# Kernel optimization log

Hardware: AMD Instinct MI355X
Metric: run time of the kernel (lower is better)

Reference implementation:

```python
import jax, jax.numpy as jnp
import numpy as np

NUM_PROJS = 7
BLOCK_SIZE = 256   # key block size
SAMPLE_SIZE = 256  # residual sampled keys


def _gray_perm(n):
    # AngularLSH._unit_hamming_distance_array: Gray-code bucket permutation
    a = np.array([0, 1], dtype=np.int32)
    for i in range(1, n):
        a = np.concatenate([a, a[::-1] + 2 ** i])
    return a

PERM = jnp.asarray(_gray_perm(NUM_PROJS))
ENC = jnp.asarray(2 ** np.arange(NUM_PROJS), dtype=jnp.int32)


def lsh_hash(x, proj_dir):
    # sign-bit angular LSH -> Gray-code bucket id, [B,H,N]
    bits = (jnp.einsum('bhnd,dr->bhnr', x, proj_dir) > 0).astype(jnp.int32)
    return PERM[(bits * ENC).sum(-1)]


def exact_attention(q, k, v, scale, bias=None):
    s = jnp.einsum('...qd,...kd->...qk', q, k) * scale
    if bias is not None:
        s = s + bias
    lse = jax.nn.logsumexp(s, axis=-1, keepdims=True)
    attn = jnp.einsum('...qk,...kd->...qd', jnp.exp(s - lse), v)
    return attn, lse


def add_self_attentions(a1, l1, a2, l2):
    # stable online-softmax combination of two attention partials
    c = jax.nn.sigmoid(l1 - l2)  # = exp(l1)/(exp(l1)+exp(l2))
    return c * a1 + (1.0 - c) * a2, jnp.logaddexp(l1, l2)


def gather_seq(x, idx):
    # x: [B,H,N,D], idx: [B,H,S] -> [B,H,S,D]
    return jnp.take_along_axis(x, idx[..., None], axis=2)


def hyper_attention(query, key, value, proj_dir, sampled_set):
    B, H, Nq, D = query.shape
    Nk = key.shape[2]
    scale = D ** -0.5
    # --- LSH bucket sort of queries and keys (stable, matches torch.sort stable=True) ---
    q_idx = jnp.argsort(lsh_hash(query, proj_dir), axis=2, stable=True)
    k_idx = jnp.argsort(lsh_hash(key, proj_dir), axis=2, stable=True)
    q_idx_inv = jnp.argsort(q_idx, axis=2, stable=True)
    q_s = gather_seq(query, q_idx)
    k_s = gather_seq(key, k_idx)
    v_s = gather_seq(value, k_idx)
    # --- block-diagonal attention over LSH-sorted blocks ---
    nb = Nk // BLOCK_SIZE          # 32 blocks
    qbs = Nq // nb                 # query block size (== 256 here)
    attn_b, lse_b = exact_attention(
        q_s.reshape(B, H, nb, qbs, D),
        k_s.reshape(B, H, nb, BLOCK_SIZE, D),
        v_s.reshape(B, H, nb, BLOCK_SIZE, D),
        scale)
    attn_b = attn_b.reshape(B, H, Nq, D)
    lse_b = lse_b.reshape(B, H, Nq, 1)
    # --- residual: uniformly sampled keys, importance weight Nk/SAMPLE_SIZE ---
    k_sub = gather_seq(k_s, sampled_set)
    v_sub = gather_seq(v_s, sampled_set)
    q_pos = jnp.arange(Nq) // qbs                    # [Nq] query block ids
    s_blk = sampled_set // BLOCK_SIZE                # [B,H,S] sampled key block ids
    overlap = q_pos[None, None, :, None] == s_blk[:, :, None, :]  # [B,H,Nq,S]
    bias = jnp.where(overlap, jnp.finfo(query.dtype).min, 0.0).astype(query.dtype)
    attn_r, lse_r = exact_attention(q_s, k_sub, v_sub, scale, bias)
    lse_r = lse_r + jnp.asarray(np.log(Nk / SAMPLE_SIZE), lse_r.dtype)
    # --- combine partials via online LSE, then unsort queries ---
    attn, lse = add_self_attentions(attn_b, lse_b, attn_r, lse_r)
    attn = gather_seq(attn, q_idx_inv)
    return attn


def setup_inputs() -> dict:
    key = jax.random.key(0)
    kq, kk, kv, kp, ks = jax.random.split(key, 5)
    B, H, N, D = 2, 16, 8192, 64
    return {
        'query': jax.random.normal(kq, (B, H, N, D), jnp.float32),
        'key': jax.random.normal(kk, (B, H, N, D), jnp.float32),
        'value': jax.random.normal(kv, (B, H, N, D), jnp.float32),
        'proj_dir': jax.random.normal(kp, (D, NUM_PROJS), jnp.float32),
        'sampled_set': jax.random.randint(ks, (B, H, SAMPLE_SIZE), 0, N),
    }


def reference(query, key, value, proj_dir, sampled_set):
    return hyper_attention(query, key, value, proj_dir, sampled_set)
```

## Files before the change

### kernel.cpp

```cpp
#include <hip/hip_runtime.h>

#define BHX   32
#define NSEQ  8192
#define NMASK 8191
#define DIM   64
#define NPROJ 7
#define NBUCK 128
#define NBLK  32
#define QBS   256
#define SSIZE 256
#define KPAD  72
#define QSC   0.18033688f

typedef unsigned short u16;
typedef unsigned int   u32;
typedef unsigned char  u8;
typedef __attribute__((ext_vector_type(8))) short bf16x8;
typedef __attribute__((ext_vector_type(4))) float f32x4;

union B8U { u32 u[4]; bf16x8 v; };

__device__ __forceinline__ u16 f2bf(float f){
    u32 u = __float_as_uint(f);
    u32 r = u + 0x7fffu + ((u >> 16) & 1u);
    return (u16)(r >> 16);
}
__device__ __forceinline__ u32 pk2(float a, float b){
    return (u32)f2bf(a) | ((u32)f2bf(b) << 16);
}
__device__ __forceinline__ f32x4 mfma16(bf16x8 a, bf16x8 b, f32x4 c){
    return __builtin_amdgcn_mfma_f32_16x16x32_bf16(a, b, c, 0, 0, 0);
}

__global__ __launch_bounds__(256) void hash_kernel(
    const float* __restrict__ qg, const float* __restrict__ kg,
    const float* __restrict__ projg,
    u8* __restrict__ bkt)
{
    const int slab = blockIdx.x, bh = blockIdx.y, tz = blockIdx.z;
    const float* __restrict__ x = tz ? kg : qg;
    u8* __restrict__ ob = bkt + ((size_t)tz * BHX + bh) * NSEQ;

    __shared__ float projs[NPROJ][DIM];
    const int t = threadIdx.x;
    if (t < 112) {
        #pragma unroll
        for (int u = 0; u < 4; u++) {
            int e = t * 4 + u;
            projs[e % NPROJ][e / NPROJ] = projg[e];
        }
    }
    __syncthreads();

    const size_t bhN = (size_t)bh * NSEQ;
    #pragma unroll
    for (int j = 0; j < 4; j++) {
        int n = slab * 1024 + j * 256 + t;
        const float4* row = (const float4*)(x + (bhN + n) * DIM);
        float dot[NPROJ];
        #pragma unroll
        for (int r = 0; r < NPROJ; r++) dot[r] = 0.0f;
        #pragma unroll
        for (int c = 0; c < 16; c++) {
            float4 wv = row[c];
            #pragma unroll
            for (int r = 0; r < NPROJ; r++) {
                float4 p = *(const float4*)&projs[r][c * 4];
                dot[r] += wv.x * p.x;
                dot[r] += wv.y * p.y;
                dot[r] += wv.z * p.z;
                dot[r] += wv.w * p.w;
            }
        }
        int code = 0;
        #pragma unroll
        for (int r = 0; r < NPROJ; r++) code |= (dot[r] > 0.0f ? 1 : 0) << r;
        ob[n] = (u8)(code ^ (code >> 1));
    }
}

__global__ __launch_bounds__(256) void sort_kernel(
    const u8* __restrict__ bkt,
    u16* __restrict__ qidx, u16* __restrict__ kidx)
{
    const int bh = blockIdx.x, tz = blockIdx.y;
    const u8* __restrict__ ib = bkt + ((size_t)tz * BHX + bh) * NSEQ;
    u16* __restrict__ idx = (tz ? kidx : qidx) + (size_t)bh * NSEQ;

    __shared__ u8  lb[NSEQ];
    __shared__ u16 hist[NBUCK][258];
    __shared__ int base[NBUCK];
    __shared__ int tot[NBUCK];

    const int t = threadIdx.x;
    {
        const uint4* src = (const uint4*)ib;
        uint4* dst = (uint4*)lb;
        dst[t] = src[t];
        dst[256 + t] = src[256 + t];
    }
    u32* hz = (u32*)&hist[0][0];
    for (int z = t; z < (NBUCK * 258) / 2; z += 256) hz[z] = 0u;
    __syncthreads();

    #pragma unroll 4
    for (int i = 0; i < 32; i++) hist[lb[t * 32 + i]][t]++;
    __syncthreads();

    if (t < NBUCK) {
        u32* hrow = (u32*)&hist[t][0];
        u32 run = 0;
        #pragma unroll 8
        for (int c = 0; c < 128; c++) {
            u32 v = hrow[c];
            u32 lo = v & 0xffffu, hi = v >> 16;
            hrow[c] = run | ((run + lo) << 16);
            run += lo + hi;
        }
        tot[t] = (int)run;
    }
    __syncthreads();

    if (t < 64) {
        int a = tot[2 * t], b = tot[2 * t + 1];
        int s = a + b;
        #pragma unroll
        for (int d = 1; d < 64; d <<= 1) {
            int v = __shfl_up(s, d);
            if (t >= d) s += v;
        }
        int excl = s - (a + b);
        base[2 * t]     = excl;
        base[2 * t + 1] = excl + a;
    }
    __syncthreads();

    #pragma unroll 4
    for (int i = 0; i < 32; i++) {
        int n = t * 32 + i;
        int b = lb[n];
        int pos = base[b] + hist[b][t];
        hist[b][t]++;
        idx[pos] = (u16)n;
    }
}

__global__ __launch_bounds__(256, 2) void attn_mfma(
    const float* __restrict__ qg, const float* __restrict__ kg,
    const float* __restrict__ vg,
    const u16* __restrict__ qidx, const u16* __restrict__ kidx,
    const int* __restrict__ samp,
    float* __restrict__ outg)
{
    __shared__ u16  Ks[64 * KPAD];
    __shared__ u16  Vt[64 * KPAD];
    __shared__ float addv[64];

    const int qb = blockIdx.x, bh = blockIdx.y, t = threadIdx.x;
    const int w = t >> 6, lane = t & 63, c = lane & 15, g = lane >> 4;
    const size_t bhN = (size_t)bh * NSEQ;

    int qi[4];
    bf16x8 qf[4][2];
    #pragma unroll
    for (int qt = 0; qt < 4; qt++) {
        qi[qt] = ((int)qidx[bhN + qb * QBS + w * 64 + qt * 16 + c]) & NMASK;
        const float* qr = qg + (bhN + (size_t)qi[qt]) * DIM;
        #pragma unroll
        for (int dk = 0; dk < 2; dk++) {
            int d0 = dk * 32 + g * 8;
            float4 xx = *(const float4*)(qr + d0);
            float4 yy = *(const float4*)(qr + d0 + 4);
            B8U f;
            f.u[0] = pk2(xx.x * QSC, xx.y * QSC);
            f.u[1] = pk2(xx.z * QSC, xx.w * QSC);
            f.u[2] = pk2(yy.x * QSC, yy.y * QSC);
            f.u[3] = pk2(yy.z * QSC, yy.w * QSC);
            qf[qt][dk] = f.v;
        }
    }

    f32x4 O[4][4];
    #pragma unroll
    for (int dt = 0; dt < 4; dt++)
        #pragma unroll
        for (int qt = 0; qt < 4; qt++) O[dt][qt] = (f32x4)0.0f;
    float m[4] = {-1e30f, -1e30f, -1e30f, -1e30f};
    float l[4] = {0.0f, 0.0f, 0.0f, 0.0f};

    const int ks_row = t >> 2, ks_q = t & 3;
    const int kp = ((ks_row >> 5) << 5) | (((ks_row >> 2) & 3) << 3)
                 | (((ks_row >> 4) & 1) << 2) | (ks_row & 3);
    const int vs_p = t & 31, vs_seg = (t >> 5) * 8;

    #pragma unroll 1
    for (int cc = 0; cc < 8; cc++) {
        __syncthreads();
        {
            int grow; float add;
            if (cc < 4) {
                grow = ((int)kidx[bhN + qb * QBS + cc * 64 + kp]) & NMASK;
                add  = 0.0f;
            } else {
                int sidx = samp[bh * SSIZE + (cc - 4) * 64 + kp] & NMASK;
                grow = ((int)kidx[bhN + sidx]) & NMASK;
                add  = ((sidx >> 8) == qb) ? -1e30f : 5.0f;
            }
            const float4* kr = (const float4*)(kg + (bhN + (size_t)grow) * DIM + ks_q * 16);
            float4 ak = kr[0], bk = kr[1], ck = kr[2], ek = kr[3];
            u32* dst = (u32*)&Ks[ks_row * KPAD + ks_q * 16];
            dst[0] = pk2(ak.x, ak.y); dst[1] = pk2(ak.z, ak.w);
            dst[2] = pk2(bk.x, bk.y); dst[3] = pk2(bk.z, bk.w);
            dst[4] = pk2(ck.x, ck.y); dst[5] = pk2(ck.z, ck.w);
            dst[6] = pk2(ek.x, ek.y); dst[7] = pk2(ek.z, ek.w);
            if (ks_q == 0) addv[ks_row] = add;

            int n0 = 2 * vs_p, n1 = n0 + 1;
            int g0, g1;
            if (cc < 4) {
                g0 = ((int)kidx[bhN + qb * QBS + cc * 64 + n0]) & NMASK;
                g1 = ((int)kidx[bhN + qb * QBS + cc * 64 + n1]) & NMASK;
            } else {
                int s0 = samp[bh * SSIZE + (cc - 4) * 64 + n0] & NMASK;
                int s1 = samp[bh * SSIZE + (cc - 4) * 64 + n1] & NMASK;
                g0 = ((int)kidx[bhN + s0]) & NMASK;
                g1 = ((int)kidx[bhN + s1]) & NMASK;
            }
            const float4* v0 = (const float4*)(vg + (bhN + (size_t)g0) * DIM + vs_seg);
            const float4* v1 = (const float4*)(vg + (bhN + (size_t)g1) * DIM + vs_seg);
            float4 a0 = v0[0], b0 = v0[1];
            float4 a1 = v1[0], b1 = v1[1];
            float va[8] = {a0.x, a0.y, a0.z, a0.w, b0.x, b0.y, b0.z, b0.w};
            float vb[8] = {a1.x, a1.y, a1.z, a1.w, b1.x, b1.y, b1.z, b1.w};
            u32* vtu = (u32*)Vt;
            #pragma unroll
            for (int i = 0; i < 8; i++)
                vtu[(vs_seg + i) * (KPAD / 2) + vs_p] = pk2(va[i], vb[i]);
        }
        __syncthreads();

        f32x4 addn[4];
        #pragma unroll
        for (int kt = 0; kt < 4; kt++)
            addn[kt] = *(const f32x4*)&addv[kt * 16 + g * 4];

        bf16x8 ka[4][2];
        #pragma unroll
        for (int kt = 0; kt < 4; kt++)
            #pragma unroll
            for (int dd = 0; dd < 2; dd++)
                ka[kt][dd] = *(const bf16x8*)&Ks[(kt * 16 + c) * KPAD + dd * 32 + g * 8];

        bf16x8 vfr[2][4];
        #pragma unroll
        for (int kk = 0; kk < 2; kk++)
            #pragma unroll
            for (int dt = 0; dt < 4; dt++)
                vfr[kk][dt] = *(const bf16x8*)&Vt[(dt * 16 + c) * KPAD + kk * 32 + g * 8];

        #pragma unroll
        for (int qt = 0; qt < 4; qt++) {
            f32x4 S[4];
            #pragma unroll
            for (int kt = 0; kt < 4; kt++) {
                S[kt] = (f32x4)0.0f;
                S[kt] = mfma16(ka[kt][0], qf[qt][0], S[kt]);
                S[kt] = mfma16(ka[kt][1], qf[qt][1], S[kt]);
                S[kt] += addn[kt];
            }
            float cmax = -1e30f;
            #pragma unroll
            for (int kt = 0; kt < 4; kt++)
                #pragma unroll
                for (int r = 0; r < 4; r++)
                    cmax = fmaxf(cmax, S[kt][r]);
            cmax = fmaxf(cmax, __shfl_xor(cmax, 16));
            cmax = fmaxf(cmax, __shfl_xor(cmax, 32));
            float mnew  = fmaxf(m[qt], cmax);
            float alpha = __builtin_exp2f(m[qt] - mnew);
            m[qt] = mnew;
            float lsum = 0.0f;
            u32 pp[4][2];
            #pragma unroll
            for (int kt = 0; kt < 4; kt++) {
                float p0 = __builtin_exp2f(S[kt][0] - mnew);
                float p1 = __builtin_exp2f(S[kt][1] - mnew);
                float p2 = __builtin_exp2f(S[kt][2] - mnew);
                float p3 = __builtin_exp2f(S[kt][3] - mnew);
                lsum += (p0 + p1) + (p2 + p3);
                pp[kt][0] = pk2(p0, p1);
                pp[kt][1] = pk2(p2, p3);
            }
            lsum += __shfl_xor(lsum, 16);
            lsum += __shfl_xor(lsum, 32);
            l[qt] = l[qt] * alpha + lsum;
            #pragma unroll
            for (int dt = 0; dt < 4; dt++) O[dt][qt] *= alpha;

            #pragma unroll
            for (int kk = 0; kk < 2; kk++) {
                B8U pf;
                pf.u[0] = pp[2 * kk][0];
                pf.u[1] = pp[2 * kk][1];
                pf.u[2] = pp[2 * kk + 1][0];
                pf.u[3] = pp[2 * kk + 1][1];
                #pragma unroll
                for (int dt = 0; dt < 4; dt++)
                    O[dt][qt] = mfma16(vfr[kk][dt], pf.v, O[dt][qt]);
            }
        }
    }

    #pragma unroll
    for (int qt = 0; qt < 4; qt++) {
        float inv = 1.0f / fmaxf(l[qt], 1e-30f);
        float* orow = outg + (bhN + (size_t)qi[qt]) * DIM;
        #pragma unroll
        for (int dt = 0; dt < 4; dt++) {
            f32x4 o = O[dt][qt] * inv;
            *(f32x4*)(orow + dt * 16 + g * 4) = o;
        }
    }
}

extern "C" void kernel_launch(void* const* d_in, const int* in_sizes, int n_in,
                              void* d_out, int out_size, void* d_ws, size_t ws_size,
                              hipStream_t stream)
{
    const float* qg   = (const float*)d_in[0];
    const float* kg   = (const float*)d_in[1];
    const float* vg   = (const float*)d_in[2];
    const float* pg   = (const float*)d_in[3];
    const int*   samp = (const int*)d_in[4];
    float* outg = (float*)d_out;

    u16* qidx = (u16*)d_ws;
    u16* kidx = qidx + BHX * NSEQ;
    u8*  bkt  = (u8*)(kidx + BHX * NSEQ);

    hipLaunchKernelGGL(hash_kernel, dim3(8, BHX, 2), dim3(256), 0, stream,
                       qg, kg, pg, bkt);
    hipLaunchKernelGGL(sort_kernel, dim3(BHX, 2), dim3(256), 0, stream,
                       bkt, qidx, kidx);
    hipLaunchKernelGGL(attn_mfma, dim3(NBLK, BHX), dim3(256), 0, stream,
                       qg, kg, vg, qidx, kidx, samp, outg);
}
```

Measured before the change: 337.2 us.

## Prefetch next K/V chunk into registers, use hardware bf16 pack, skip rescale

```diff
diff --git a/kernel.cpp b/kernel.cpp
--- a/kernel.cpp
+++ b/kernel.cpp
@@ -20,13 +20,10 @@
 
 union B8U { u32 u[4]; bf16x8 v; };
 
-__device__ __forceinline__ u16 f2bf(float f){
-    u32 u = __float_as_uint(f);
-    u32 r = u + 0x7fffu + ((u >> 16) & 1u);
-    return (u16)(r >> 16);
-}
-__device__ __forceinline__ u32 pk2(float a, float b){
-    return (u32)f2bf(a) | ((u32)f2bf(b) << 16);
+__device__ __forceinline__ u32 cpk(float a, float b){
+    u32 r;
+    asm("v_cvt_pk_bf16_f32 %0, %1, %2" : "=v"(r) : "v"(a), "v"(b));
+    return r;
 }
 __device__ __forceinline__ f32x4 mfma16(bf16x8 a, bf16x8 b, f32x4 c){
     return __builtin_amdgcn_mfma_f32_16x16x32_bf16(a, b, c, 0, 0, 0);
@@ -172,10 +169,10 @@
             float4 xx = *(const float4*)(qr + d0);
             float4 yy = *(const float4*)(qr + d0 + 4);
             B8U f;
-            f.u[0] = pk2(xx.x * QSC, xx.y * QSC);
-            f.u[1] = pk2(xx.z * QSC, xx.w * QSC);
-            f.u[2] = pk2(yy.x * QSC, yy.y * QSC);
-            f.u[3] = pk2(yy.z * QSC, yy.w * QSC);
+            f.u[0] = cpk(xx.x * QSC, xx.y * QSC);
+            f.u[1] = cpk(xx.z * QSC, xx.w * QSC);
+            f.u[2] = cpk(yy.x * QSC, yy.y * QSC);
+            f.u[3] = cpk(yy.z * QSC, yy.w * QSC);
             qf[qt][dk] = f.v;
         }
     }
@@ -193,51 +190,59 @@
                  | (((ks_row >> 4) & 1) << 2) | (ks_row & 3);
     const int vs_p = t & 31, vs_seg = (t >> 5) * 8;
 
+    float4 kA, kB, kC, kD;
+    float4 vA, vB, vC, vD;
+    float  padd;
+
+    auto prefetch = [&](int cc) {
+        int grow;
+        if (cc < 4) {
+            grow = ((int)kidx[bhN + qb * QBS + cc * 64 + kp]) & NMASK;
+            padd = 0.0f;
+        } else {
+            int sidx = samp[bh * SSIZE + (cc - 4) * 64 + kp] & NMASK;
+            grow = ((int)kidx[bhN + sidx]) & NMASK;
+            padd = ((sidx >> 8) == qb) ? -1e30f : 5.0f;
+        }
+        const float4* kr = (const float4*)(kg + (bhN + (size_t)grow) * DIM + ks_q * 16);
+        kA = kr[0]; kB = kr[1]; kC = kr[2]; kD = kr[3];
+        int n0 = 2 * vs_p, n1 = n0 + 1, g0, g1;
+        if (cc < 4) {
+            g0 = ((int)kidx[bhN + qb * QBS + cc * 64 + n0]) & NMASK;
+            g1 = ((int)kidx[bhN + qb * QBS + cc * 64 + n1]) & NMASK;
+        } else {
+            int s0 = samp[bh * SSIZE + (cc - 4) * 64 + n0] & NMASK;
+            int s1 = samp[bh * SSIZE + (cc - 4) * 64 + n1] & NMASK;
+            g0 = ((int)kidx[bhN + s0]) & NMASK;
+            g1 = ((int)kidx[bhN + s1]) & NMASK;
+        }
+        const float4* v0 = (const float4*)(vg + (bhN + (size_t)g0) * DIM + vs_seg);
+        const float4* v1 = (const float4*)(vg + (bhN + (size_t)g1) * DIM + vs_seg);
+        vA = v0[0]; vB = v0[1]; vC = v1[0]; vD = v1[1];
+    };
+
+    prefetch(0);
+
     #pragma unroll 1
     for (int cc = 0; cc < 8; cc++) {
         __syncthreads();
         {
-            int grow; float add;
-            if (cc < 4) {
-                grow = ((int)kidx[bhN + qb * QBS + cc * 64 + kp]) & NMASK;
-                add  = 0.0f;
-            } else {
-                int sidx = samp[bh * SSIZE + (cc - 4) * 64 + kp] & NMASK;
-                grow = ((int)kidx[bhN + sidx]) & NMASK;
-                add  = ((sidx >> 8) == qb) ? -1e30f : 5.0f;
-            }
-            const float4* kr = (const float4*)(kg + (bhN + (size_t)grow) * DIM + ks_q * 16);
-            float4 ak = kr[0], bk = kr[1], ck = kr[2], ek = kr[3];
             u32* dst = (u32*)&Ks[ks_row * KPAD + ks_q * 16];
-            dst[0] = pk2(ak.x, ak.y); dst[1] = pk2(ak.z, ak.w);
-            dst[2] = pk2(bk.x, bk.y); dst[3] = pk2(bk.z, bk.w);
-            dst[4] = pk2(ck.x, ck.y); dst[5] = pk2(ck.z, ck.w);
-            dst[6] = pk2(ek.x, ek.y); dst[7] = pk2(ek.z, ek.w);
-            if (ks_q == 0) addv[ks_row] = add;
-
-            int n0 = 2 * vs_p, n1 = n0 + 1;
-            int g0, g1;
-            if (cc < 4) {
-                g0 = ((int)kidx[bhN + qb * QBS + cc * 64 + n0]) & NMASK;
-                g1 = ((int)kidx[bhN + qb * QBS + cc * 64 + n1]) & NMASK;
-            } else {
-                int s0 = samp[bh * SSIZE + (cc - 4) * 64 + n0] & NMASK;
-                int s1 = samp[bh * SSIZE + (cc - 4) * 64 + n1] & NMASK;
-                g0 = ((int)kidx[bhN + s0]) & NMASK;
-                g1 = ((int)kidx[bhN + s1]) & NMASK;
-            }
-            const float4* v0 = (const float4*)(vg + (bhN + (size_t)g0) * DIM + vs_seg);
-            const float4* v1 = (const float4*)(vg + (bhN + (size_t)g1) * DIM + vs_seg);
-            float4 a0 = v0[0], b0 = v0[1];
-            float4 a1 = v1[0], b1 = v1[1];
-            float va[8] = {a0.x, a0.y, a0.z, a0.w, b0.x, b0.y, b0.z, b0.w};
-            float vb[8] = {a1.x, a1.y, a1.z, a1.w, b1.x, b1.y, b1.z, b1.w};
+            dst[0] = cpk(kA.x, kA.y); dst[1] = cpk(kA.z, kA.w);
+            dst[2] = cpk(kB.x, kB.y); dst[3] = cpk(kB.z, kB.w);
+            dst[4] = cpk(kC.x, kC.y); dst[5] = cpk(kC.z, kC.w);
+            dst[6] = cpk(kD.x, kD.y); dst[7] = cpk(kD.z, kD.w);
+            if (ks_q == 0) addv[ks_row] = padd;
+            float va[8] = {vA.x, vA.y, vA.z, vA.w, vB.x, vB.y, vB.z, vB.w};
+            float vb[8] = {vC.x, vC.y, vC.z, vC.w, vD.x, vD.y, vD.z, vD.w};
             u32* vtu = (u32*)Vt;
             #pragma unroll
             for (int i = 0; i < 8; i++)
-                vtu[(vs_seg + i) * (KPAD / 2) + vs_p] = pk2(va[i], vb[i]);
+                vtu[(vs_seg + i) * (KPAD / 2) + vs_p] = cpk(va[i], vb[i]);
         }
         __syncthreads();
+
+        if (cc < 7) prefetch(cc + 1);
 
         f32x4 addn[4];
         #pragma unroll
@@ -263,10 +268,8 @@
             f32x4 S[4];
             #pragma unroll
             for (int kt = 0; kt < 4; kt++) {
-                S[kt] = (f32x4)0.0f;
-                S[kt] = mfma16(ka[kt][0], qf[qt][0], S[kt]);
+                S[kt] = mfma16(ka[kt][0], qf[qt][0], addn[kt]);
                 S[kt] = mfma16(ka[kt][1], qf[qt][1], S[kt]);
-                S[kt] += addn[kt];
             }
             float cmax = -1e30f;
             #pragma unroll
@@ -276,26 +279,30 @@
                     cmax = fmaxf(cmax, S[kt][r]);
             cmax = fmaxf(cmax, __shfl_xor(cmax, 16));
             cmax = fmaxf(cmax, __shfl_xor(cmax, 32));
-            float mnew  = fmaxf(m[qt], cmax);
-            float alpha = __builtin_exp2f(m[qt] - mnew);
-            m[qt] = mnew;
+            if (__any(cmax > m[qt])) {
+                float mnew  = fmaxf(m[qt], cmax);
+                float alpha = __builtin_exp2f(m[qt] - mnew);
+                m[qt] = mnew;
+                l[qt] *= alpha;
+                #pragma unroll
+                for (int dt = 0; dt < 4; dt++) O[dt][qt] *= alpha;
+            }
+            const float mq = m[qt];
             float lsum = 0.0f;
             u32 pp[4][2];
             #pragma unroll
             for (int kt = 0; kt < 4; kt++) {
-                float p0 = __builtin_exp2f(S[kt][0] - mnew);
-                float p1 = __builtin_exp2f(S[kt][1] - mnew);
-                float p2 = __builtin_exp2f(S[kt][2] - mnew);
-                float p3 = __builtin_exp2f(S[kt][3] - mnew);
+                float p0 = __builtin_exp2f(S[kt][0] - mq);
+                float p1 = __builtin_exp2f(S[kt][1] - mq);
+                float p2 = __builtin_exp2f(S[kt][2] - mq);
+                float p3 = __builtin_exp2f(S[kt][3] - mq);
                 lsum += (p0 + p1) + (p2 + p3);
-                pp[kt][0] = pk2(p0, p1);
-                pp[kt][1] = pk2(p2, p3);
+                pp[kt][0] = cpk(p0, p1);
+                pp[kt][1] = cpk(p2, p3);
             }
             lsum += __shfl_xor(lsum, 16);
             lsum += __shfl_xor(lsum, 32);
-            l[qt] = l[qt] * alpha + lsum;
-            #pragma unroll
-            for (int dt = 0; dt < 4; dt++) O[dt][qt] *= alpha;
+            l[qt] += lsum;
 
             #pragma unroll
             for (int kk = 0; kk < 2; kk++) {
```

Measured after the change: 324.1 us. 3.9% less time.
